# Kernel optimization log

Measured on AMD Instinct MI355X. Metric: run time of the kernel, lower is better.

The kernel has to match this reference:

```python
import jax, jax.numpy as jnp
import numpy as np

M, N, K, C, H = 100000, 8192, 32, 256, 8
DH = C // H
FF = 512
R = (15, 15, 7)  # 2*MAXRANGE-1 per axis for MAXRANGE=[8,8,4]


def _layer_norm(x, g, b, eps=1e-5):
    mu = jnp.mean(x, axis=-1, keepdims=True)
    xc = x - mu
    var = jnp.mean(xc * xc, axis=-1, keepdims=True)
    return xc * jax.lax.rsqrt(var + eps) * g + b


def setup_inputs() -> dict:
    key = jax.random.key(0)
    ks = iter(jax.random.split(key, 40))
    d = {}
    d['voxel_features'] = jax.random.normal(next(ks), (M, C), jnp.float32)
    d['query_coords'] = jax.random.normal(next(ks), (N, 3), jnp.float32)
    d['query_indices'] = jax.random.randint(next(ks), (N,), 0, M)
    d['gather_indices'] = jax.random.randint(next(ks), (N, K), 0, M)
    d['gather_mask'] = jax.random.randint(next(ks), (N, K), 0, 2).astype(bool)
    d['rel_x'] = jax.random.randint(next(ks), (N, K), 0, R[0])
    d['rel_y'] = jax.random.randint(next(ks), (N, K), 0, R[1])
    d['rel_z'] = jax.random.randint(next(ks), (N, K), 0, R[2])
    s = 0.02
    # pos_proj: Conv1d(3, C, 1) == linear on coords
    d['w_pos'] = jax.random.normal(next(ks), (3, C), jnp.float32) * s
    d['b_pos'] = jnp.zeros((C,), jnp.float32)
    for nm in ['q', 'k', 'v', 'proj']:
        d['w_' + nm] = jax.random.normal(next(ks), (C, C), jnp.float32) * (C ** -0.5)
        d['b_' + nm] = jnp.zeros((C,), jnp.float32)
    d['ln1_g'] = jnp.ones((C,), jnp.float32); d['ln1_b'] = jnp.zeros((C,), jnp.float32)
    d['ln2_g'] = jnp.ones((C,), jnp.float32); d['ln2_b'] = jnp.zeros((C,), jnp.float32)
    d['w_ff1'] = jax.random.normal(next(ks), (C, FF), jnp.float32) * (C ** -0.5)
    d['b_ff1'] = jnp.zeros((FF,), jnp.float32)
    d['w_ff2'] = jax.random.normal(next(ks), (FF, C), jnp.float32) * (FF ** -0.5)
    d['b_ff2'] = jnp.zeros((C,), jnp.float32)
    # per-axis relative position tables: [H, DH, 2W-1] for q-side and k-side
    for m in ['q', 'k']:
        for ax, r in zip(['x', 'y', 'z'], R):
            d[f'pos_{m}{ax}'] = jax.random.normal(next(ks), (H, DH, r), jnp.float32) * s
    return d


def reference(voxel_features, query_coords, query_indices, gather_indices, gather_mask,
              rel_x, rel_y, rel_z,
              w_pos, b_pos, w_q, b_q, w_k, b_k, w_v, b_v, w_proj, b_proj,
              ln1_g, ln1_b, ln2_g, ln2_b, w_ff1, b_ff1, w_ff2, b_ff2,
              pos_qx, pos_qy, pos_qz, pos_kx, pos_ky, pos_kz):
    x = _layer_norm(voxel_features, ln1_g, ln1_b)           # [M, C] pre-norm
    # gather window centers (queries) + positional projection of coords
    q_in = x[query_indices] + jax.nn.relu(query_coords @ w_pos + b_pos)  # [N, C]
    kv_in = x[gather_indices]                                # [N, K, C]
    kv_in = jnp.where(gather_mask[..., None], 0.0, kv_in)
    q = (q_in @ w_q + b_q).reshape(N, H, DH)
    k = (kv_in @ w_k + b_k).reshape(N, K, H, DH)
    v = (kv_in @ w_v + b_v).reshape(N, K, H, DH)
    logits = jnp.einsum('nhd,nkhd->nhk', q, k) * (DH ** -0.5)  # [N, H, K]
    # query-side per-axis relative position bias: contract q with table, gather at rel idx
    for pos, rel in ((pos_qx, rel_x), (pos_qy, rel_y), (pos_qz, rel_z)):
        qp = jnp.einsum('nhd,hdr->nhr', q, pos)              # [N, H, R]
        logits = logits + jnp.take_along_axis(qp, rel[:, None, :], axis=2)
    # key-side per-axis relative position bias
    for pos, rel in ((pos_kx, rel_x), (pos_ky, rel_y), (pos_kz, rel_z)):
        kp = jnp.einsum('nkhd,hdr->nkhr', k, pos)            # [N, K, H, R]
        bias = jnp.take_along_axis(kp, rel[:, :, None, None], axis=3)[..., 0]  # [N, K, H]
        logits = logits + bias.transpose(0, 2, 1)
    logits = jnp.where(gather_mask[:, None, :], -1e9, logits)
    attn = jax.nn.softmax(logits, axis=-1)
    out = jnp.einsum('nhk,nkhd->nhd', attn, v).reshape(N, C) @ w_proj + b_proj
    act = voxel_features[query_indices] + out                # residual (pre-norm block)
    h = jax.nn.relu(_layer_norm(act, ln2_g, ln2_b) @ w_ff1 + b_ff1) @ w_ff2 + b_ff2
    return act + h                                           # [N, C]
```

## Files before the change

### kernel.cpp

```cpp
#include <hip/hip_runtime.h>
#include <hip/hip_bf16.h>
#include <math.h>

#define MV   100000
#define NQ   8192
#define KN   32
#define CH   256
#define NH   8
#define DHD  32
#define FFD  512
#define NG   (NQ*KN)
#define QPW  37
#define QPN  (NH*QPW)
#define ASTR 40

typedef __bf16 bf16x8 __attribute__((ext_vector_type(8)));
typedef float  f32x4  __attribute__((ext_vector_type(4)));

__device__ __forceinline__ float bf2f(unsigned short u) {
    return __uint_as_float(((unsigned int)u) << 16);
}
__device__ __forceinline__ unsigned short f2bf(float f) {
    unsigned int x = __float_as_uint(f);
    unsigned int r = x + 0x7FFFu + ((x >> 16) & 1u);
    return (unsigned short)(r >> 16);
}
__device__ __forceinline__ void glds16(const unsigned short* g, unsigned short* l) {
    __builtin_amdgcn_global_load_lds(
        (const __attribute__((address_space(1))) void*)g,
        (__attribute__((address_space(3))) void*)l, 16, 0, 0);
}

__global__ __launch_bounds__(256) void k_detect_mask(const unsigned char* __restrict__ raw,
                                                     int* __restrict__ flags) {
    __shared__ int any;
    if (threadIdx.x == 0) any = 0;
    __syncthreads();
    const uint4* p = (const uint4*)raw;
    int i = blockIdx.x * 256 + threadIdx.x;
    uint4 v = p[i];
    if ((v.x | v.y | v.z | v.w) & 0xFFFFFF00u) any = 1;
    __syncthreads();
    if (threadIdx.x == 0) flags[blockIdx.x] = any;
}

__global__ __launch_bounds__(256) void k_prep(const float* __restrict__ w_k,
                                              const float* __restrict__ w_v,
                                              const float* __restrict__ w_ff1,
                                              const float* __restrict__ w_ff2,
                                              const float* __restrict__ w_proj,
                                              const float* __restrict__ b_k,
                                              const float* __restrict__ b_v,
                                              const void* __restrict__ mask_raw,
                                              const int* __restrict__ flags,
                                              unsigned short* __restrict__ w_kv_t,
                                              unsigned short* __restrict__ w1_t,
                                              unsigned short* __restrict__ w2_t,
                                              unsigned short* __restrict__ wp_t,
                                              float* __restrict__ bkv,
                                              int* __restrict__ mask_i) {
    __shared__ int bl;
    if (threadIdx.x == 0) {
        int a = 0;
        #pragma unroll 8
        for (int i = 0; i < 64; i++) a |= flags[i];
        bl = a;
    }
    __syncthreads();
    int byteLayout = bl;
    int idx = blockIdx.x * 256 + threadIdx.x;
    if (blockIdx.x == 0 && threadIdx.x < 512)
        bkv[threadIdx.x] = (threadIdx.x < 256) ? b_k[threadIdx.x]
                                               : b_v[threadIdx.x - 256];
    if (idx < NG) {
        int mv = byteLayout ? (int)((const unsigned char*)mask_raw)[idx]
                            : ((const int*)mask_raw)[idx];
        mask_i[idx] = (mv != 0) ? 1 : 0;
    }
    if (idx < 512 * 256) {
        int col = idx >> 8, j = idx & 255;
        float v = (col < 256) ? w_k[j * 256 + col] : w_v[j * 256 + (col - 256)];
        w_kv_t[idx] = f2bf(v);
    }
    if (idx < 512 * 256) {
        int n = idx >> 8, k = idx & 255;
        w1_t[idx] = f2bf(w_ff1[k * FFD + n]);
    }
    if (idx < 256 * 512) {
        int n = idx >> 9, k = idx & 511;
        w2_t[idx] = f2bf(w_ff2[k * CH + n]);
    }
    if (idx < 256 * 256) {
        int n = idx >> 8, k = idx & 255;
        wp_t[idx] = f2bf(w_proj[k * CH + n]);
    }
}

__global__ __launch_bounds__(256) void k_posc(const float* __restrict__ pos_kx,
                                              const float* __restrict__ pos_ky,
                                              const float* __restrict__ pos_kz,
                                              float* __restrict__ comb) {
    int idx = blockIdx.x * 256 + threadIdx.x;
    if (idx >= 8 * 15 * 15 * 7 * 32) return;
    int d = idx & 31, r = idx >> 5;
    int rz = r % 7;  r /= 7;
    int ry = r % 15; r /= 15;
    int rx = r % 15; int h = r / 15;
    comb[idx] = pos_kx[(h * DHD + d) * 15 + rx]
              + pos_ky[(h * DHD + d) * 15 + ry]
              + pos_kz[(h * DHD + d) * 7  + rz];
}

__global__ __launch_bounds__(256) void k_ln(const float* __restrict__ x,
                                            const float* __restrict__ g,
                                            const float* __restrict__ b,
                                            unsigned short* __restrict__ o,
                                            int nrows) {
    int wid = threadIdx.x >> 6, lane = threadIdx.x & 63;
    int row = blockIdx.x * 4 + wid;
    if (row >= nrows) return;
    const float4 v = *(const float4*)(x + (size_t)row * CH + lane * 4);
    float s  = v.x + v.y + v.z + v.w;
    float sq = v.x * v.x + v.y * v.y + v.z * v.z + v.w * v.w;
    #pragma unroll
    for (int off = 1; off < 64; off <<= 1) {
        s  += __shfl_xor(s,  off);
        sq += __shfl_xor(sq, off);
    }
    float mu  = s * (1.f / CH);
    float var = sq * (1.f / CH) - mu * mu;
    float rs  = rsqrtf(var + 1e-5f);
    float4 gv = *(const float4*)(g + lane * 4);
    float4 bv = *(const float4*)(b + lane * 4);
    ushort4 ov;
    ov.x = f2bf((v.x - mu) * rs * gv.x + bv.x);
    ov.y = f2bf((v.y - mu) * rs * gv.y + bv.y);
    ov.z = f2bf((v.z - mu) * rs * gv.z + bv.z);
    ov.w = f2bf((v.w - mu) * rs * gv.w + bv.w);
    *(ushort4*)(o + (size_t)row * CH + lane * 4) = ov;
}

__global__ __launch_bounds__(256) void k_q(const unsigned short* __restrict__ ln_x,
                                           const float* __restrict__ coords,
                                           const int* __restrict__ qidx,
                                           const float* __restrict__ w_pos,
                                           const float* __restrict__ b_pos,
                                           const float* __restrict__ w_q,
                                           const float* __restrict__ b_q,
                                           const float* __restrict__ pos_qx,
                                           const float* __restrict__ pos_qy,
                                           const float* __restrict__ pos_qz,
                                           float* __restrict__ qout,
                                           float* __restrict__ qp) {
    __shared__ float qin_s[8 * CH];
    __shared__ float q_s[8 * CH];
    int c = threadIdx.x;
    int nb = blockIdx.x * 8;
    float wp0 = w_pos[c], wp1 = w_pos[CH + c], wp2 = w_pos[2 * CH + c], bp = b_pos[c];
    #pragma unroll
    for (int qq = 0; qq < 8; qq++) {
        int n = nb + qq;
        float p = bp + coords[n * 3] * wp0 + coords[n * 3 + 1] * wp1 + coords[n * 3 + 2] * wp2;
        p = fmaxf(p, 0.f);
        int qi = qidx[n];
        qin_s[qq * CH + c] = bf2f(ln_x[(size_t)qi * CH + c]) + p;
    }
    __syncthreads();
    float acc[8];
    float bq = b_q[c];
    #pragma unroll
    for (int qq = 0; qq < 8; qq++) acc[qq] = bq;
    #pragma unroll 4
    for (int j = 0; j < CH; j++) {
        float w = w_q[j * CH + c];
        #pragma unroll
        for (int qq = 0; qq < 8; qq++) acc[qq] += qin_s[qq * CH + j] * w;
    }
    #pragma unroll
    for (int qq = 0; qq < 8; qq++) {
        qout[(size_t)(nb + qq) * CH + c] = acc[qq];
        q_s[qq * CH + c] = acc[qq];
    }
    __syncthreads();
    for (int t = threadIdx.x; t < 8 * QPN; t += 256) {
        int qq = t / QPN, u = t % QPN;
        int h = u / QPW, r = u % QPW;
        const float* tab; int rr, R;
        if (r < 15)      { tab = pos_qx; rr = r;      R = 15; }
        else if (r < 30) { tab = pos_qy; rr = r - 15; R = 15; }
        else             { tab = pos_qz; rr = r - 30; R = 7;  }
        float a = 0.f;
        const float* qrow = q_s + qq * CH + h * DHD;
        #pragma unroll
        for (int d = 0; d < DHD; d++) a += qrow[d] * tab[(h * DHD + d) * R + rr];
        qp[(size_t)(nb + qq) * QPN + u] = a;
    }
}

__global__ __launch_bounds__(256) void k_kv(const unsigned short* __restrict__ ln_x,
                                            const unsigned short* __restrict__ w_kv_t,
                                            const float* __restrict__ bkv,
                                            unsigned short* __restrict__ kv) {
    __shared__ __align__(16) unsigned short As[128 * 32];
    __shared__ __align__(16) unsigned short Bs[128 * 32];
    const int tid = threadIdx.x;
    const int w = tid >> 6, l = tid & 63;
    const int wr = w >> 1, wc = w & 1;
    const int rowbase = blockIdx.y * 128;
    const int col0 = blockIdx.x * 128;
    const int sr = l >> 2, sq = l & 3;
    int ra0 = rowbase + w * 16 + sr;      if (ra0 >= MV) ra0 = MV - 1;
    int ra1 = rowbase + 64 + w * 16 + sr; if (ra1 >= MV) ra1 = MV - 1;
    const unsigned short* pa0 = ln_x + (size_t)ra0 * CH + sq * 8;
    const unsigned short* pa1 = ln_x + (size_t)ra1 * CH + sq * 8;
    const unsigned short* pb0 = w_kv_t + (size_t)(col0 + w * 16 + sr) * CH + sq * 8;
    const unsigned short* pb1 = w_kv_t + (size_t)(col0 + 64 + w * 16 + sr) * CH + sq * 8;
    unsigned short* lA0 = As + w * 512;
    unsigned short* lA1 = As + 2048 + w * 512;
    unsigned short* lB0 = Bs + w * 512;
    unsigned short* lB1 = Bs + 2048 + w * 512;

    f32x4 acc[4][4];
    #pragma unroll
    for (int mt = 0; mt < 4; mt++)
        #pragma unroll
        for (int nt = 0; nt < 4; nt++)
            acc[mt][nt] = (f32x4){0.f, 0.f, 0.f, 0.f};

    const int ml = l & 15, qd = l >> 4;
    for (int kk = 0; kk < CH; kk += 32) {
        __syncthreads();
        glds16(pa0 + kk, lA0);
        glds16(pa1 + kk, lA1);
        glds16(pb0 + kk, lB0);
        glds16(pb1 + kk, lB1);
        __syncthreads();
        bf16x8 af[4], bf[4];
        #pragma unroll
        for (int mt = 0; mt < 4; mt++)
            af[mt] = *(const bf16x8*)(As + (wr * 64 + mt * 16 + ml) * 32 + qd * 8);
        #pragma unroll
        for (int nt = 0; nt < 4; nt++)
            bf[nt] = *(const bf16x8*)(Bs + (wc * 64 + nt * 16 + ml) * 32 + qd * 8);
        #pragma unroll
        for (int mt = 0; mt < 4; mt++)
            #pragma unroll
            for (int nt = 0; nt < 4; nt++)
                acc[mt][nt] = __builtin_amdgcn_mfma_f32_16x16x32_bf16(af[mt], bf[nt], acc[mt][nt], 0, 0, 0);
    }

    float bb[4];
    #pragma unroll
    for (int nt = 0; nt < 4; nt++)
        bb[nt] = bkv[col0 + wc * 64 + nt * 16 + ml];
    unsigned short* trs = As;
    #pragma unroll
    for (int mt = 0; mt < 4; mt++) {
        __syncthreads();
        #pragma unroll
        for (int nt = 0; nt < 4; nt++) {
            int lcol = wc * 64 + nt * 16 + ml;
            #pragma unroll
            for (int i = 0; i < 4; i++)
                trs[wr * 2048 + (qd * 4 + i) * 128 + lcol] = f2bf(acc[mt][nt][i] + bb[nt]);
        }
        __syncthreads();
        int rl = tid >> 4, cc = (tid & 15) * 8;
        int g0 = rowbase + mt * 16 + rl;
        int g1 = rowbase + 64 + mt * 16 + rl;
        if (g0 < MV)
            *(uint4*)(kv + (size_t)g0 * 512 + col0 + cc) = *(const uint4*)(trs + rl * 128 + cc);
        if (g1 < MV)
            *(uint4*)(kv + (size_t)g1 * 512 + col0 + cc) = *(const uint4*)(trs + 2048 + rl * 128 + cc);
    }
}

template <int KD, int EPI>
__global__ __launch_bounds__(256) void k_mm(const unsigned short* __restrict__ A,
                                            const unsigned short* __restrict__ Bt_g,
                                            const float* __restrict__ bias,
                                            const float* __restrict__ res,
                                            const int* __restrict__ qidx,
                                            unsigned short* __restrict__ out_bf,
                                            float* __restrict__ out_f) {
    __shared__ __align__(16) unsigned short As[128 * ASTR];
    __shared__ __align__(16) unsigned short Bs[64 * ASTR];
    int tid = threadIdx.x;
    int w = tid >> 6, l = tid & 63;
    int rowbase = blockIdx.y * 128;
    int col0 = blockIdx.x * 64;
    int r0 = tid >> 2, qt = tid & 3;
    const unsigned short* a0p = A + (size_t)(rowbase + r0) * KD + qt * 8;
    const unsigned short* a1p = A + (size_t)(rowbase + 64 + r0) * KD + qt * 8;

    f32x4 acc[2][4];
    #pragma unroll
    for (int mt = 0; mt < 2; mt++)
        #pragma unroll
        for (int nt = 0; nt < 4; nt++)
            acc[mt][nt] = (f32x4){0.f, 0.f, 0.f, 0.f};

    const int ml = l & 15, qd = l >> 4;
    for (int kk = 0; kk < KD; kk += 32) {
        __syncthreads();
        uint4 v0 = *(const uint4*)(a0p + kk);
        uint4 v1 = *(const uint4*)(a1p + kk);
        *(uint4*)(As + r0 * ASTR + qt * 8)        = v0;
        *(uint4*)(As + (64 + r0) * ASTR + qt * 8) = v1;
        {
            uint4 bv = *(const uint4*)(Bt_g + (size_t)(col0 + r0) * KD + kk + qt * 8);
            *(uint4*)(Bs + r0 * ASTR + qt * 8) = bv;
        }
        __syncthreads();
        bf16x8 a0 = *(const bf16x8*)(As + (w * 32 + ml) * ASTR + qd * 8);
        bf16x8 a1 = *(const bf16x8*)(As + (w * 32 + 16 + ml) * ASTR + qd * 8);
        #pragma unroll
        for (int nt = 0; nt < 4; nt++) {
            bf16x8 bb = *(const bf16x8*)(Bs + (nt * 16 + ml) * ASTR + qd * 8);
            acc[0][nt] = __builtin_amdgcn_mfma_f32_16x16x32_bf16(a0, bb, acc[0][nt], 0, 0, 0);
            acc[1][nt] = __builtin_amdgcn_mfma_f32_16x16x32_bf16(a1, bb, acc[1][nt], 0, 0, 0);
        }
    }

    #pragma unroll
    for (int nt = 0; nt < 4; nt++) {
        int col = col0 + nt * 16 + ml;
        float bv = bias[col];
        #pragma unroll
        for (int mt = 0; mt < 2; mt++) {
            int rl = w * 32 + mt * 16 + qd * 4;
            #pragma unroll
            for (int i = 0; i < 4; i++) {
                int row = rowbase + rl + i;
                float v = acc[mt][nt][i] + bv;
                if (EPI == 0) {
                    out_bf[(size_t)row * FFD + col] = f2bf(fmaxf(v, 0.f));
                } else if (EPI == 1) {
                    out_f[(size_t)row * CH + col] = v + res[(size_t)row * CH + col];
                } else {
                    int qi = qidx[row];
                    out_f[(size_t)row * CH + col] = v + res[(size_t)qi * CH + col];
                }
            }
        }
    }
}

__global__ __launch_bounds__(256) void k_attn(const float* __restrict__ qbuf,
                                              const float* __restrict__ qp,
                                              const unsigned short* __restrict__ kvmat,
                                              const int* __restrict__ gidx,
                                              const int* __restrict__ mask_i,
                                              const int* __restrict__ rel_x,
                                              const int* __restrict__ rel_y,
                                              const int* __restrict__ rel_z,
                                              const float* __restrict__ comb,
                                              float* __restrict__ attn) {
    __shared__ float q_s[1024];
    __shared__ float qp_s[4 * QPN];
    int tid = threadIdx.x;
    int qb = blockIdx.x * 4;
    for (int i = tid; i < 1024; i += 256) q_s[i] = qbuf[(size_t)qb * CH + i];
    for (int i = tid; i < 4 * QPN; i += 256) qp_s[i] = qp[(size_t)qb * QPN + i];
    __syncthreads();
    int h = tid >> 5, k = tid & 31;
    const float scale = 0.17677669529663687f;
    for (int qq = 0; qq < 4; qq++) {
        int n = qb + qq;
        int gi = n * KN + k;
        int mk = mask_i[gi];
        float lg = -1e9f;
        if (!mk) {
            int rx = rel_x[gi], ry = rel_y[gi], rz = rel_z[gi];
            int g = gidx[gi];
            const uint4* kp = (const uint4*)(kvmat + (size_t)g * 512 + h * DHD);
            float kv[32];
            #pragma unroll
            for (int j = 0; j < 4; j++) {
                uint4 u = kp[j];
                kv[j * 8 + 0] = bf2f((unsigned short)(u.x & 0xFFFF));
                kv[j * 8 + 1] = bf2f((unsigned short)(u.x >> 16));
                kv[j * 8 + 2] = bf2f((unsigned short)(u.y & 0xFFFF));
                kv[j * 8 + 3] = bf2f((unsigned short)(u.y >> 16));
                kv[j * 8 + 4] = bf2f((unsigned short)(u.z & 0xFFFF));
                kv[j * 8 + 5] = bf2f((unsigned short)(u.z >> 16));
                kv[j * 8 + 6] = bf2f((unsigned short)(u.w & 0xFFFF));
                kv[j * 8 + 7] = bf2f((unsigned short)(u.w >> 16));
            }
            const float* cp = comb + ((((h * 15 + rx) * 15 + ry) * 7 + rz) << 5);
            float s1 = 0.f, s2 = 0.f;
            const float* qrow = q_s + qq * CH + h * DHD;
            #pragma unroll
            for (int d = 0; d < 32; d++) {
                s1 += kv[d] * qrow[d];
                s2 += kv[d] * cp[d];
            }
            lg = s1 * scale + s2
               + qp_s[qq * QPN + h * QPW + rx]
               + qp_s[qq * QPN + h * QPW + 15 + ry]
               + qp_s[qq * QPN + h * QPW + 30 + rz];
        }
        float mx = lg;
        #pragma unroll
        for (int off = 1; off <= 16; off <<= 1) mx = fmaxf(mx, __shfl_xor(mx, off));
        float e = mk ? 0.f : __expf(lg - mx);
        float sm = e;
        #pragma unroll
        for (int off = 1; off <= 16; off <<= 1) sm += __shfl_xor(sm, off);
        attn[(size_t)n * 256 + tid] = (sm > 0.f) ? e / sm : 0.f;
    }
}

__global__ __launch_bounds__(256) void k_av(const unsigned short* __restrict__ kvmat,
                                            const int* __restrict__ gidx,
                                            const int* __restrict__ mask_i,
                                            const float* __restrict__ attn,
                                            const float* __restrict__ b_v,
                                            unsigned short* __restrict__ attnln) {
    __shared__ float attn_s[4 * 256];
    __shared__ int mask_s[4 * 32];
    int tid = threadIdx.x;
    int w = tid >> 6, l = tid & 63;
    int qb = blockIdx.x * 4;
    for (int i = tid; i < 1024; i += 256) attn_s[i] = attn[(size_t)qb * 256 + i];
    if (tid < 128) mask_s[tid] = mask_i[qb * 32 + tid];
    __syncthreads();
    int n = qb + w;
    int h = l >> 3;
    float a0 = 0.f, a1 = 0.f, a2 = 0.f, a3 = 0.f;
    int nm = 0;
    for (int k = 0; k < KN; k++) {
        if (mask_s[w * 32 + k]) continue;
        nm++;
        int g = gidx[n * 32 + k];
        ushort4 v4 = *(const ushort4*)(kvmat + (size_t)g * 512 + 256 + l * 4);
        float av = attn_s[w * 256 + h * 32 + k];
        a0 += av * bf2f(v4.x);
        a1 += av * bf2f(v4.y);
        a2 += av * bf2f(v4.z);
        a3 += av * bf2f(v4.w);
    }
    int col = l * 4;
    if (nm == 0) {
        a0 = b_v[col]; a1 = b_v[col + 1]; a2 = b_v[col + 2]; a3 = b_v[col + 3];
    }
    ushort4 o;
    o.x = f2bf(a0); o.y = f2bf(a1); o.z = f2bf(a2); o.w = f2bf(a3);
    *(ushort4*)(attnln + (size_t)n * CH + col) = o;
}

extern "C" void kernel_launch(void* const* d_in, const int* in_sizes, int n_in,
                              void* d_out, int out_size, void* d_ws, size_t ws_size,
                              hipStream_t stream) {
    (void)in_sizes; (void)n_in; (void)out_size; (void)ws_size;
    const float* vox    = (const float*)d_in[0];
    const float* coords = (const float*)d_in[1];
    const int*   qidx   = (const int*)d_in[2];
    const int*   gidx   = (const int*)d_in[3];
    const void*  mraw   = d_in[4];
    const int*   rel_x  = (const int*)d_in[5];
    const int*   rel_y  = (const int*)d_in[6];
    const int*   rel_z  = (const int*)d_in[7];
    const float* w_pos  = (const float*)d_in[8];
    const float* b_pos  = (const float*)d_in[9];
    const float* w_q    = (const float*)d_in[10];
    const float* b_q    = (const float*)d_in[11];
    const float* w_k    = (const float*)d_in[12];
    const float* b_k    = (const float*)d_in[13];
    const float* w_v    = (const float*)d_in[14];
    const float* b_v    = (const float*)d_in[15];
    const float* w_proj = (const float*)d_in[16];
    const float* b_proj = (const float*)d_in[17];
    const float* ln1_g  = (const float*)d_in[18];
    const float* ln1_b  = (const float*)d_in[19];
    const float* ln2_g  = (const float*)d_in[20];
    const float* ln2_b  = (const float*)d_in[21];
    const float* w_ff1  = (const float*)d_in[22];
    const float* b_ff1  = (const float*)d_in[23];
    const float* w_ff2  = (const float*)d_in[24];
    const float* b_ff2  = (const float*)d_in[25];
    const float* pos_qx = (const float*)d_in[26];
    const float* pos_qy = (const float*)d_in[27];
    const float* pos_qz = (const float*)d_in[28];
    const float* pos_kx = (const float*)d_in[29];
    const float* pos_ky = (const float*)d_in[30];
    const float* pos_kz = (const float*)d_in[31];

    char* p = (char*)d_ws;
    auto take = [&](size_t n) { char* r = p; p += (n + 255) & ~(size_t)255; return r; };
    unsigned short* ln_x    = (unsigned short*)take((size_t)MV * CH * 2);
    unsigned short* w_kv_t  = (unsigned short*)take((size_t)512 * 256 * 2);
    unsigned short* w1_t    = (unsigned short*)take((size_t)512 * 256 * 2);
    unsigned short* w2_t    = (unsigned short*)take((size_t)256 * 512 * 2);
    unsigned short* wp_t    = (unsigned short*)take((size_t)256 * 256 * 2);
    float*          bkv     = (float*)take(512 * 4);
    int*            flags   = (int*)take(64 * 4);
    int*            mask_i  = (int*)take((size_t)NG * 4);
    float*          comb    = (float*)take((size_t)8 * 15 * 15 * 7 * 32 * 4);
    float*          qbuf    = (float*)take((size_t)NQ * CH * 4);
    float*          qp      = (float*)take((size_t)NQ * QPN * 4);
    unsigned short* kvmat   = (unsigned short*)take((size_t)MV * 512 * 2);
    float*          attn    = (float*)take((size_t)NQ * 256 * 4);
    unsigned short* attnln  = (unsigned short*)take((size_t)NQ * CH * 2);
    float*          actbuf  = (float*)take((size_t)NQ * CH * 4);
    unsigned short* actln   = (unsigned short*)take((size_t)NQ * CH * 2);
    unsigned short* hbuf    = (unsigned short*)take((size_t)NQ * FFD * 2);

    hipLaunchKernelGGL(k_detect_mask, dim3(64), dim3(256), 0, stream,
                       (const unsigned char*)mraw, flags);
    hipLaunchKernelGGL(k_prep, dim3(NG / 256), dim3(256), 0, stream,
                       w_k, w_v, w_ff1, w_ff2, w_proj, b_k, b_v, mraw, flags,
                       w_kv_t, w1_t, w2_t, wp_t, bkv, mask_i);
    hipLaunchKernelGGL(k_posc, dim3((8 * 15 * 15 * 7 * 32 + 255) / 256), dim3(256), 0, stream,
                       pos_kx, pos_ky, pos_kz, comb);
    hipLaunchKernelGGL(k_ln, dim3(MV / 4 + 1), dim3(256), 0, stream,
                       vox, ln1_g, ln1_b, ln_x, MV);
    hipLaunchKernelGGL(k_q, dim3(NQ / 8), dim3(256), 0, stream,
                       ln_x, coords, qidx, w_pos, b_pos, w_q, b_q,
                       pos_qx, pos_qy, pos_qz, qbuf, qp);
    hipLaunchKernelGGL(k_kv, dim3(4, (MV + 127) / 128), dim3(256), 0, stream,
                       ln_x, w_kv_t, bkv, kvmat);
    hipLaunchKernelGGL(k_attn, dim3(NQ / 4), dim3(256), 0, stream,
                       qbuf, qp, kvmat, gidx, mask_i, rel_x, rel_y, rel_z, comb, attn);
    hipLaunchKernelGGL(k_av, dim3(NQ / 4), dim3(256), 0, stream,
                       kvmat, gidx, mask_i, attn, b_v, attnln);
    hipLaunchKernelGGL(HIP_KERNEL_NAME(k_mm<256, 2>), dim3(4, NQ / 128), dim3(256), 0, stream,
                       attnln, wp_t, b_proj, vox, qidx,
                       (unsigned short*)nullptr, actbuf);
    hipLaunchKernelGGL(k_ln, dim3(NQ / 4), dim3(256), 0, stream,
                       actbuf, ln2_g, ln2_b, actln, NQ);
    hipLaunchKernelGGL(HIP_KERNEL_NAME(k_mm<256, 0>), dim3(8, NQ / 128), dim3(256), 0, stream,
                       actln, w1_t, b_ff1, (const float*)nullptr, (const int*)nullptr,
                       hbuf, (float*)nullptr);
    hipLaunchKernelGGL(HIP_KERNEL_NAME(k_mm<512, 1>), dim3(4, NQ / 128), dim3(256), 0, stream,
                       hbuf, w2_t, b_ff2, actbuf, (const int*)nullptr,
                       (unsigned short*)nullptr, (float*)d_out);
}
```

Measured before the change: 456.8 us.

## Move query projection and query-position bias onto bf16 MFMA GEMMs

Replaces the scalar fp32 k_q kernel with a gather-only k_qin kernel and two bf16 MFMA GEMM launches. The first computes q from a transposed bf16 w_q. The second computes the query-side position bias as a GEMM against a block-diagonal padded table (QPL=320 columns) built in the prep kernel. This removes slow per-thread FMA loops and a scalar dot-product pass. In exchange it adds bf16 rounding to q and the bias, wasted work on the zero blocks of the diagonal table, and extra launches.

```diff
diff --git a/kernel.cpp b/kernel.cpp
--- a/kernel.cpp
+++ b/kernel.cpp
@@ -12,6 +12,7 @@
 #define NG   (NQ*KN)
 #define QPW  37
 #define QPN  (NH*QPW)
+#define QPL  320
 #define ASTR 40
 
 typedef __bf16 bf16x8 __attribute__((ext_vector_type(8)));
@@ -49,15 +50,22 @@
                                               const float* __restrict__ w_ff1,
                                               const float* __restrict__ w_ff2,
                                               const float* __restrict__ w_proj,
+                                              const float* __restrict__ w_q,
                                               const float* __restrict__ b_k,
                                               const float* __restrict__ b_v,
+                                              const float* __restrict__ pos_qx,
+                                              const float* __restrict__ pos_qy,
+                                              const float* __restrict__ pos_qz,
                                               const void* __restrict__ mask_raw,
                                               const int* __restrict__ flags,
                                               unsigned short* __restrict__ w_kv_t,
                                               unsigned short* __restrict__ w1_t,
                                               unsigned short* __restrict__ w2_t,
                                               unsigned short* __restrict__ wp_t,
+                                              unsigned short* __restrict__ wq_t,
+                                              unsigned short* __restrict__ wqp_t,
                                               float* __restrict__ bkv,
+                                              float* __restrict__ zbias,
                                               int* __restrict__ mask_i) {
     __shared__ int bl;
     if (threadIdx.x == 0) {
@@ -72,6 +80,7 @@
     if (blockIdx.x == 0 && threadIdx.x < 512)
         bkv[threadIdx.x] = (threadIdx.x < 256) ? b_k[threadIdx.x]
                                                : b_v[threadIdx.x - 256];
+    if (idx < QPL) zbias[idx] = 0.f;
     if (idx < NG) {
         int mv = byteLayout ? (int)((const unsigned char*)mask_raw)[idx]
                             : ((const int*)mask_raw)[idx];
@@ -93,6 +102,21 @@
     if (idx < 256 * 256) {
         int n = idx >> 8, k = idx & 255;
         wp_t[idx] = f2bf(w_proj[k * CH + n]);
+        wq_t[idx] = f2bf(w_q[k * CH + n]);
+    }
+    if (idx < QPL * 256) {
+        int col = idx >> 8, k = idx & 255;
+        float v = 0.f;
+        if (col < QPN) {
+            int h = col / QPW, r = col % QPW;
+            int h2 = k >> 5, d = k & 31;
+            if (h2 == h) {
+                if (r < 15)      v = pos_qx[(h * DHD + d) * 15 + r];
+                else if (r < 30) v = pos_qy[(h * DHD + d) * 15 + (r - 15)];
+                else             v = pos_qz[(h * DHD + d) * 7  + (r - 30)];
+            }
+        }
+        wqp_t[idx] = f2bf(v);
     }
 }
 
@@ -140,20 +164,12 @@
     *(ushort4*)(o + (size_t)row * CH + lane * 4) = ov;
 }
 
-__global__ __launch_bounds__(256) void k_q(const unsigned short* __restrict__ ln_x,
-                                           const float* __restrict__ coords,
-                                           const int* __restrict__ qidx,
-                                           const float* __restrict__ w_pos,
-                                           const float* __restrict__ b_pos,
-                                           const float* __restrict__ w_q,
-                                           const float* __restrict__ b_q,
-                                           const float* __restrict__ pos_qx,
-                                           const float* __restrict__ pos_qy,
-                                           const float* __restrict__ pos_qz,
-                                           float* __restrict__ qout,
-                                           float* __restrict__ qp) {
-    __shared__ float qin_s[8 * CH];
-    __shared__ float q_s[8 * CH];
+__global__ __launch_bounds__(256) void k_qin(const unsigned short* __restrict__ ln_x,
+                                             const float* __restrict__ coords,
+                                             const int* __restrict__ qidx,
+                                             const float* __restrict__ w_pos,
+                                             const float* __restrict__ b_pos,
+                                             unsigned short* __restrict__ qin) {
     int c = threadIdx.x;
     int nb = blockIdx.x * 8;
     float wp0 = w_pos[c], wp1 = w_pos[CH + c], wp2 = w_pos[2 * CH + c], bp = b_pos[c];
@@ -163,37 +179,7 @@
         float p = bp + coords[n * 3] * wp0 + coords[n * 3 + 1] * wp1 + coords[n * 3 + 2] * wp2;
         p = fmaxf(p, 0.f);
         int qi = qidx[n];
-        qin_s[qq * CH + c] = bf2f(ln_x[(size_t)qi * CH + c]) + p;
-    }
-    __syncthreads();
-    float acc[8];
-    float bq = b_q[c];
-    #pragma unroll
-    for (int qq = 0; qq < 8; qq++) acc[qq] = bq;
-    #pragma unroll 4
-    for (int j = 0; j < CH; j++) {
-        float w = w_q[j * CH + c];
-        #pragma unroll
-        for (int qq = 0; qq < 8; qq++) acc[qq] += qin_s[qq * CH + j] * w;
-    }
-    #pragma unroll
-    for (int qq = 0; qq < 8; qq++) {
-        qout[(size_t)(nb + qq) * CH + c] = acc[qq];
-        q_s[qq * CH + c] = acc[qq];
-    }
-    __syncthreads();
-    for (int t = threadIdx.x; t < 8 * QPN; t += 256) {
-        int qq = t / QPN, u = t % QPN;
-        int h = u / QPW, r = u % QPW;
-        const float* tab; int rr, R;
-        if (r < 15)      { tab = pos_qx; rr = r;      R = 15; }
-        else if (r < 30) { tab = pos_qy; rr = r - 15; R = 15; }
-        else             { tab = pos_qz; rr = r - 30; R = 7;  }
-        float a = 0.f;
-        const float* qrow = q_s + qq * CH + h * DHD;
-        #pragma unroll
-        for (int d = 0; d < DHD; d++) a += qrow[d] * tab[(h * DHD + d) * R + rr];
-        qp[(size_t)(nb + qq) * QPN + u] = a;
+        qin[(size_t)n * CH + c] = f2bf(bf2f(ln_x[(size_t)qi * CH + c]) + p);
     }
 }
 
@@ -275,7 +261,7 @@
     }
 }
 
-template <int KD, int EPI>
+template <int KD, int EPI, int LDO>
 __global__ __launch_bounds__(256) void k_mm(const unsigned short* __restrict__ A,
                                             const unsigned short* __restrict__ Bt_g,
                                             const float* __restrict__ bias,
@@ -334,12 +320,17 @@
                 int row = rowbase + rl + i;
                 float v = acc[mt][nt][i] + bv;
                 if (EPI == 0) {
-                    out_bf[(size_t)row * FFD + col] = f2bf(fmaxf(v, 0.f));
+                    out_bf[(size_t)row * LDO + col] = f2bf(fmaxf(v, 0.f));
                 } else if (EPI == 1) {
                     out_f[(size_t)row * CH + col] = v + res[(size_t)row * CH + col];
-                } else {
+                } else if (EPI == 2) {
                     int qi = qidx[row];
                     out_f[(size_t)row * CH + col] = v + res[(size_t)qi * CH + col];
+                } else if (EPI == 3) {
+                    out_f[(size_t)row * CH + col] = v;
+                    out_bf[(size_t)row * CH + col] = f2bf(v);
+                } else {
+                    out_f[(size_t)row * LDO + col] = v;
                 }
             }
         }
@@ -357,11 +348,11 @@
                                               const float* __restrict__ comb,
                                               float* __restrict__ attn) {
     __shared__ float q_s[1024];
-    __shared__ float qp_s[4 * QPN];
+    __shared__ float qp_s[4 * QPL];
     int tid = threadIdx.x;
     int qb = blockIdx.x * 4;
     for (int i = tid; i < 1024; i += 256) q_s[i] = qbuf[(size_t)qb * CH + i];
-    for (int i = tid; i < 4 * QPN; i += 256) qp_s[i] = qp[(size_t)qb * QPN + i];
+    for (int i = tid; i < 4 * QPL; i += 256) qp_s[i] = qp[(size_t)qb * QPL + i];
     __syncthreads();
     int h = tid >> 5, k = tid & 31;
     const float scale = 0.17677669529663687f;
@@ -396,9 +387,9 @@
                 s2 += kv[d] * cp[d];
             }
             lg = s1 * scale + s2
-               + qp_s[qq * QPN + h * QPW + rx]
-               + qp_s[qq * QPN + h * QPW + 15 + ry]
-               + qp_s[qq * QPN + h * QPW + 30 + rz];
+               + qp_s[qq * QPL + h * QPW + rx]
+               + qp_s[qq * QPL + h * QPW + 15 + ry]
+               + qp_s[qq * QPL + h * QPW + 30 + rz];
         }
         float mx = lg;
         #pragma unroll
@@ -493,12 +484,17 @@
     unsigned short* w1_t    = (unsigned short*)take((size_t)512 * 256 * 2);
     unsigned short* w2_t    = (unsigned short*)take((size_t)256 * 512 * 2);
     unsigned short* wp_t    = (unsigned short*)take((size_t)256 * 256 * 2);
+    unsigned short* wq_t    = (unsigned short*)take((size_t)256 * 256 * 2);
+    unsigned short* wqp_t   = (unsigned short*)take((size_t)QPL * 256 * 2);
     float*          bkv     = (float*)take(512 * 4);
+    float*          zbias   = (float*)take(QPL * 4);
     int*            flags   = (int*)take(64 * 4);
     int*            mask_i  = (int*)take((size_t)NG * 4);
     float*          comb    = (float*)take((size_t)8 * 15 * 15 * 7 * 32 * 4);
+    unsigned short* qin     = (unsigned short*)take((size_t)NQ * CH * 2);
     float*          qbuf    = (float*)take((size_t)NQ * CH * 4);
-    float*          qp      = (float*)take((size_t)NQ * QPN * 4);
+    unsigned short* qbf     = (unsigned short*)take((size_t)NQ * CH * 2);
+    float*          qp      = (float*)take((size_t)NQ * QPL * 4);
     unsigned short* kvmat   = (unsigned short*)take((size_t)MV * 512 * 2);
     float*          attn    = (float*)take((size_t)NQ * 256 * 4);
     unsigned short* attnln  = (unsigned short*)take((size_t)NQ * CH * 2);
@@ -509,30 +505,36 @@
     hipLaunchKernelGGL(k_detect_mask, dim3(64), dim3(256), 0, stream,
                        (const unsigned char*)mraw, flags);
     hipLaunchKernelGGL(k_prep, dim3(NG / 256), dim3(256), 0, stream,
-                       w_k, w_v, w_ff1, w_ff2, w_proj, b_k, b_v, mraw, flags,
-                       w_kv_t, w1_t, w2_t, wp_t, bkv, mask_i);
+                       w_k, w_v, w_ff1, w_ff2, w_proj, w_q, b_k, b_v,
+                       pos_qx, pos_qy, pos_qz, mraw, flags,
+                       w_kv_t, w1_t, w2_t, wp_t, wq_t, wqp_t, bkv, zbias, mask_i);
     hipLaunchKernelGGL(k_posc, dim3((8 * 15 * 15 * 7 * 32 + 255) / 256), dim3(256), 0, stream,
                        pos_kx, pos_ky, pos_kz, comb);
     hipLaunchKernelGGL(k_ln, dim3(MV / 4 + 1), dim3(256), 0, stream,
                        vox, ln1_g, ln1_b, ln_x, MV);
-    hipLaunchKernelGGL(k_q, dim3(NQ / 8), dim3(256), 0, stream,
-                       ln_x, coords, qidx, w_pos, b_pos, w_q, b_q,
-                       pos_qx, pos_qy, pos_qz, qbuf, qp);
+    hipLaunchKernelGGL(k_qin, dim3(NQ / 8), dim3(256), 0, stream,
+                       ln_x, coords, qidx, w_pos, b_pos, qin);
     hipLaunchKernelGGL(k_kv, dim3(4, (MV + 127) / 128), dim3(256), 0, stream,
                        ln_x, w_kv_t, bkv, kvmat);
+    hipLaunchKernelGGL(HIP_KERNEL_NAME(k_mm<256, 3, CH>), dim3(4, NQ / 128), dim3(256), 0, stream,
+                       qin, wq_t, b_q, (const float*)nullptr, (const int*)nullptr,
+                       qbf, qbuf);
+    hipLaunchKernelGGL(HIP_KERNEL_NAME(k_mm<256, 4, QPL>), dim3(QPL / 64, NQ / 128), dim3(256), 0, stream,
+                       qbf, wqp_t, zbias, (const float*)nullptr, (const int*)nullptr,
+                       (unsigned short*)nullptr, qp);
     hipLaunchKernelGGL(k_attn, dim3(NQ / 4), dim3(256), 0, stream,
                        qbuf, qp, kvmat, gidx, mask_i, rel_x, rel_y, rel_z, comb, attn);
     hipLaunchKernelGGL(k_av, dim3(NQ / 4), dim3(256), 0, stream,
                        kvmat, gidx, mask_i, attn, b_v, attnln);
-    hipLaunchKernelGGL(HIP_KERNEL_NAME(k_mm<256, 2>), dim3(4, NQ / 128), dim3(256), 0, stream,
+    hipLaunchKernelGGL(HIP_KERNEL_NAME(k_mm<256, 2, CH>), dim3(4, NQ / 128), dim3(256), 0, stream,
                        attnln, wp_t, b_proj, vox, qidx,
                        (unsigned short*)nullptr, actbuf);
     hipLaunchKernelGGL(k_ln, dim3(NQ / 4), dim3(256), 0, stream,
                        actbuf, ln2_g, ln2_b, actln, NQ);
-    hipLaunchKernelGGL(HIP_KERNEL_NAME(k_mm<256, 0>), dim3(8, NQ / 128), dim3(256), 0, stream,
+    hipLaunchKernelGGL(HIP_KERNEL_NAME(k_mm<256, 0, FFD>), dim3(8, NQ / 128), dim3(256), 0, stream,
                        actln, w1_t, b_ff1, (const float*)nullptr, (const int*)nullptr,
                        hbuf, (float*)nullptr);
-    hipLaunchKernelGGL(HIP_KERNEL_NAME(k_mm<512, 1>), dim3(4, NQ / 128), dim3(256), 0, stream,
+    hipLaunchKernelGGL(HIP_KERNEL_NAME(k_mm<512, 1, CH>), dim3(4, NQ / 128), dim3(256), 0, stream,
                        hbuf, w2_t, b_ff2, actbuf, (const int*)nullptr,
                        (unsigned short*)nullptr, (float*)d_out);
 }
```

New measurement: 406.3 us. -11.1%, faster.
